# Kernel tuning notes

Measured on AMD Instinct MI355X. Metric: run time of the kernel, lower is better.

The kernel has to match this reference:

```python
import jax, jax.numpy as jnp
import numpy as np

EMBED_DIM = 1024
NUM_HEADS = 16
HEAD_DIM = EMBED_DIM // NUM_HEADS
B, N = 4, 2048


def setup_inputs() -> dict:
    key = jax.random.key(0)
    k = jax.random.split(key, 5)
    scale = 1.0 / np.sqrt(EMBED_DIM)
    return {
        "x": jax.random.normal(k[0], (B, N, EMBED_DIM), dtype=jnp.float32),
        # torch nn.Linear convention: y = x @ W.T + b, W shape [out, in]
        "qkv_w": jax.random.uniform(k[1], (3 * EMBED_DIM, EMBED_DIM), jnp.float32, -scale, scale),
        "qkv_b": jax.random.uniform(k[2], (3 * EMBED_DIM,), jnp.float32, -scale, scale),
        "out_w": jax.random.uniform(k[3], (EMBED_DIM, EMBED_DIM), jnp.float32, -scale, scale),
        "out_b": jax.random.uniform(k[4], (EMBED_DIM,), jnp.float32, -scale, scale),
    }


def reference(x, qkv_w, qkv_b, out_w, out_b):
    b, n, e = x.shape
    qkv = x @ qkv_w.T + qkv_b                      # [B,N,3E]
    qkv = qkv.reshape(b, n, 3, NUM_HEADS, HEAD_DIM)
    qkv = jnp.transpose(qkv, (2, 0, 3, 1, 4))      # [3,B,H,N,D]
    q, k, v = qkv[0], qkv[1], qkv[2]
    scores = jnp.einsum("bhqd,bhkd->bhqk", q, k) / np.sqrt(HEAD_DIM)
    weights = jax.nn.softmax(scores, axis=-1)
    attn = jnp.einsum("bhqk,bhkd->bhqd", weights, v)  # [B,H,N,D]
    attn = jnp.transpose(attn, (0, 2, 1, 3)).reshape(b, n, e)
    return attn @ out_w.T + out_b
```

## Files before the change

### kernel.cpp

```cpp
#include <hip/hip_runtime.h>
#include <hip/hip_bf16.h>

#define EMBED 1024
#define NHEADS 16
#define HDIM 64
#define BATCH 4
#define SEQ 2048
#define MROWS (BATCH*SEQ)
#define QKVN (3*EMBED)
#define KDIM 1024

typedef __bf16 bf16;
typedef __bf16 bf16x4 __attribute__((ext_vector_type(4)));
typedef __bf16 bf16x8 __attribute__((ext_vector_type(8)));
typedef float f32x4 __attribute__((ext_vector_type(4)));
typedef float f32x16 __attribute__((ext_vector_type(16)));

#define QSCALE 0.18033688011112042f

#define NX (MROWS*EMBED/4)
#define NQ (QKVN*KDIM/4)
#define NO (EMBED*KDIM/4)
__global__ void cvt_all(const float* __restrict__ x, const float* __restrict__ qw,
                        const float* __restrict__ ow,
                        bf16* __restrict__ xb, bf16* __restrict__ qwb, bf16* __restrict__ owb) {
    int i = blockIdx.x * blockDim.x + threadIdx.x;
    const float* src; bf16* dst; int j;
    if (i < NX)            { src = x;  dst = xb;  j = i; }
    else if (i < NX + NQ)  { src = qw; dst = qwb; j = i - NX; }
    else if (i < NX+NQ+NO) { src = ow; dst = owb; j = i - NX - NQ; }
    else return;
    float4 f = ((const float4*)src)[j];
    bf16x4 o;
    o[0] = (bf16)f.x; o[1] = (bf16)f.y; o[2] = (bf16)f.z; o[3] = (bf16)f.w;
    *((bf16x4*)dst + j) = o;
}

template<int MODE>
__launch_bounds__(256)
__global__ void gemm_bt(const bf16* __restrict__ A, const bf16* __restrict__ B,
                        const float* __restrict__ bias,
                        float* __restrict__ outF,
                        bf16* __restrict__ Qb, bf16* __restrict__ Kb, bf16* __restrict__ Vt)
{
    __shared__ __align__(16) char ldsmem[16384];
    bf16 (*Alds)[32] = (bf16(*)[32])ldsmem;
    bf16 (*Blds)[32] = (bf16(*)[32])(ldsmem + 8192);
    bf16* bounce = (bf16*)ldsmem;

    const int tid = threadIdx.x;
    const int l = tid & 63, w = tid >> 6;
    const int wr = w >> 1, wc = w & 1;
    const int tM = blockIdx.y * 128, tN = blockIdx.x * 128;

    f32x4 acc[4][4] = {};
    const bf16* Abase = A + (size_t)tM * KDIM;
    const bf16* Bbase = B + (size_t)tN * KDIM;

    for (int k0 = 0; k0 < KDIM; k0 += 32) {
        #pragma unroll
        for (int t = 0; t < 2; ++t) {
            int idx = t * 256 + tid;
            int row = idx >> 2;
            int kc = (idx & 3) * 8;
            __builtin_amdgcn_global_load_lds(
                (const __attribute__((address_space(1))) void*)(Abase + (size_t)row * KDIM + k0 + kc),
                (__attribute__((address_space(3))) void*)((char*)&Alds[0][0] + idx * 16),
                16, 0, 0);
            __builtin_amdgcn_global_load_lds(
                (const __attribute__((address_space(1))) void*)(Bbase + (size_t)row * KDIM + k0 + kc),
                (__attribute__((address_space(3))) void*)((char*)&Blds[0][0] + idx * 16),
                16, 0, 0);
        }
        __syncthreads();
        bf16x8 a[4], b[4];
        #pragma unroll
        for (int i = 0; i < 4; ++i)
            a[i] = *(const bf16x8*)&Alds[wr * 64 + i * 16 + (l & 15)][(l >> 4) * 8];
        #pragma unroll
        for (int j = 0; j < 4; ++j)
            b[j] = *(const bf16x8*)&Blds[wc * 64 + j * 16 + (l & 15)][(l >> 4) * 8];
        #pragma unroll
        for (int i = 0; i < 4; ++i)
            #pragma unroll
            for (int j = 0; j < 4; ++j)
                acc[i][j] = __builtin_amdgcn_mfma_f32_16x16x32_bf16(a[i], b[j], acc[i][j], 0, 0, 0);
        __syncthreads();
    }

    if (MODE == 1) {
        #pragma unroll
        for (int i = 0; i < 4; ++i) {
            #pragma unroll
            for (int j = 0; j < 4; ++j) {
                int n = tN + wc * 64 + j * 16 + (l & 15);
                float bv = bias[n];
                #pragma unroll
                for (int r = 0; r < 4; ++r) {
                    int m = tM + wr * 64 + i * 16 + (l >> 4) * 4 + r;
                    outF[(size_t)m * EMBED + n] = acc[i][j][r] + bv;
                }
            }
        }
    } else {
        const int which = tN >> 10;
        const int bidx  = tM >> 11;
        const int hd0   = (tN & 1023) >> 6;
        const int t32base = (tM & 2047) >> 5;
        bf16* dstbase = (which == 0) ? Qb : (which == 1) ? Kb : Vt;
        const float scale = (which == 0) ? QSCALE : 1.0f;

        float bj[4];
        #pragma unroll
        for (int j = 0; j < 4; ++j)
            bj[j] = bias[tN + wc * 64 + j * 16 + (l & 15)];

        #pragma unroll
        for (int pass = 0; pass < 2; ++pass) {
            __syncthreads();
            #pragma unroll
            for (int ii = 0; ii < 2; ++ii) {
                const int i = pass * 2 + ii;
                #pragma unroll
                for (int j = 0; j < 4; ++j) {
                    const int d = (wc * 64 + j * 16 + (l & 15)) & 63;
                    #pragma unroll
                    for (int r = 0; r < 4; ++r) {
                        const int nsl = wr * 64 + i * 16 + (l >> 4) * 4 + r;
                        float v = acc[i][j][r] + bj[j];
                        int off;
                        if (which == 2) {
                            int dblk = d >> 5;
                            int rem16 = nsl & 15;
                            int c = (nsl >> 4) & 1;
                            int fj = (rem16 & 3) | ((rem16 & 8) >> 1);
                            int fhi = (rem16 >> 2) & 1;
                            int lane = (d & 31) | (fhi << 5);
                            off = (dblk * 2 + c) * 512 + lane * 8 + fj;
                        } else {
                            int kk = d >> 4, fhi = (d >> 3) & 1, fj = d & 7;
                            int lane = (nsl & 31) | (fhi << 5);
                            off = kk * 512 + lane * 8 + fj;
                        }
                        bounce[(wc * 2 + wr) * 2048 + off] = (bf16)(v * scale);
                    }
                }
            }
            __syncthreads();
            const int chunk = tid >> 6;
            size_t gbase = ((size_t)(bidx * NHEADS + hd0 + (chunk >> 1)) * 64
                            + t32base + 2 * (chunk & 1) + pass) * 2048;
            #pragma unroll
            for (int s = 0; s < 4; ++s) {
                int eoff = s * 512 + (tid & 63) * 8;
                *(bf16x8*)(dstbase + gbase + eoff) = *(const bf16x8*)&bounce[chunk * 2048 + eoff];
            }
        }
    }
}

static __device__ __forceinline__ unsigned cvt_pk(float lo, float hi) {
    unsigned r;
    asm("v_cvt_pk_bf16_f32 %0, %1, %2" : "=v"(r) : "v"(lo), "v"(hi));
    return r;
}

__launch_bounds__(256)
__global__ void attn_kernel(const bf16* __restrict__ Qb, const bf16* __restrict__ Kb,
                            const bf16* __restrict__ Vt, bf16* __restrict__ AO)
{
    const int tid = threadIdx.x, l = tid & 63, w = tid >> 6;
    const int lo5 = l & 31, hi = l >> 5;
    int bid = blockIdx.x;
    int swz = (bid & 7) * 128 + (bid >> 3);
    const int bh = swz >> 4;
    const int qt = swz & 15;

    const bf16* QFh = Qb + (size_t)bh * (64 * 2048);
    const bf16* Kit = Kb + (size_t)bh * (64 * 2048) + (size_t)l * 8;
    const bf16* Vit = Vt + (size_t)bh * (64 * 2048) + (size_t)l * 8;

    const int qtile = qt * 4 + w;
    const bf16* qbase = QFh + (size_t)qtile * 2048 + (size_t)l * 8;
    bf16x8 qf[4];
    #pragma unroll
    for (int kk = 0; kk < 4; ++kk)
        qf[kk] = *(const bf16x8*)(qbase + kk * 512);

    f32x16 O0 = {}, O1 = {};
    float lsum = 0.f;

    bf16x8 vA00 = *(const bf16x8*)(Vit);
    bf16x8 vA01 = *(const bf16x8*)(Vit + 512);
    bf16x8 vA10 = *(const bf16x8*)(Vit + 1024);
    bf16x8 vA11 = *(const bf16x8*)(Vit + 1536);
    bf16x8 vB00, vB01, vB10, vB11;

    bf16x8 kK0 = *(const bf16x8*)(Kit);
    bf16x8 kK1 = *(const bf16x8*)(Kit + 512);
    bf16x8 kK2 = *(const bf16x8*)(Kit + 1024);
    bf16x8 kK3 = *(const bf16x8*)(Kit + 1536);

    f32x16 SA, SB;
    #pragma unroll
    for (int r = 0; r < 16; ++r) SA[r] = 0.f;
    SA = __builtin_amdgcn_mfma_f32_32x32x16_bf16(kK0, qf[0], SA, 0, 0, 0);
    SA = __builtin_amdgcn_mfma_f32_32x32x16_bf16(kK1, qf[1], SA, 0, 0, 0);
    SA = __builtin_amdgcn_mfma_f32_32x32x16_bf16(kK2, qf[2], SA, 0, 0, 0);
    SA = __builtin_amdgcn_mfma_f32_32x32x16_bf16(kK3, qf[3], SA, 0, 0, 0);
    kK0 = *(const bf16x8*)(Kit + 2048);
    kK1 = *(const bf16x8*)(Kit + 2048 + 512);
    kK2 = *(const bf16x8*)(Kit + 2048 + 1024);
    kK3 = *(const bf16x8*)(Kit + 2048 + 1536);

#define ATTN_BODY(T, SCUR, SNXT, VC00, VC01, VC10, VC11, VN00, VN01, VN10, VN11)        \
    {                                                                                    \
        const int t = (T);                                                               \
        int tv = t + 1; tv = (tv < 64) ? tv : 0;                                         \
        const bf16* vb = Vit + (size_t)tv * 2048;                                        \
        VN00 = *(const bf16x8*)(vb);                                                     \
        VN01 = *(const bf16x8*)(vb + 512);                                               \
        VN10 = *(const bf16x8*)(vb + 1024);                                              \
        VN11 = *(const bf16x8*)(vb + 1536);                                              \
        __builtin_amdgcn_s_setprio(1);                                                   \
        _Pragma("unroll")                                                                \
        for (int r = 0; r < 16; ++r) SNXT[r] = 0.f;                                      \
        SNXT = __builtin_amdgcn_mfma_f32_32x32x16_bf16(kK0, qf[0], SNXT, 0, 0, 0);       \
        SNXT = __builtin_amdgcn_mfma_f32_32x32x16_bf16(kK1, qf[1], SNXT, 0, 0, 0);       \
        SNXT = __builtin_amdgcn_mfma_f32_32x32x16_bf16(kK2, qf[2], SNXT, 0, 0, 0);       \
        SNXT = __builtin_amdgcn_mfma_f32_32x32x16_bf16(kK3, qf[3], SNXT, 0, 0, 0);       \
        __builtin_amdgcn_s_setprio(0);                                                   \
        int tp = t + 2; tp = (tp < 64) ? tp : 0;                                         \
        const bf16* kb = Kit + (size_t)tp * 2048;                                        \
        kK0 = *(const bf16x8*)(kb);                                                      \
        kK1 = *(const bf16x8*)(kb + 512);                                                \
        kK2 = *(const bf16x8*)(kb + 1024);                                               \
        kK3 = *(const bf16x8*)(kb + 1536);                                               \
        float p[16];                                                                     \
        _Pragma("unroll")                                                                \
        for (int r = 0; r < 16; ++r)                                                     \
            p[r] = __builtin_amdgcn_exp2f(SCUR[r]);                                      \
        float s0 = (p[0] + p[1]) + (p[2] + p[3]);                                        \
        float s1 = (p[4] + p[5]) + (p[6] + p[7]);                                        \
        float s2 = (p[8] + p[9]) + (p[10] + p[11]);                                      \
        float s3 = (p[12] + p[13]) + (p[14] + p[15]);                                    \
        lsum += (s0 + s1) + (s2 + s3);                                                   \
        union { unsigned u[4]; bf16x8 v; } pk0, pk1;                                     \
        pk0.u[0] = cvt_pk(p[0], p[1]);   pk0.u[1] = cvt_pk(p[2], p[3]);                  \
        pk0.u[2] = cvt_pk(p[4], p[5]);   pk0.u[3] = cvt_pk(p[6], p[7]);                  \
        pk1.u[0] = cvt_pk(p[8], p[9]);   pk1.u[1] = cvt_pk(p[10], p[11]);                \
        pk1.u[2] = cvt_pk(p[12], p[13]); pk1.u[3] = cvt_pk(p[14], p[15]);                \
        __builtin_amdgcn_s_setprio(1);                                                   \
        O0 = __builtin_amdgcn_mfma_f32_32x32x16_bf16(VC00, pk0.v, O0, 0, 0, 0);          \
        O0 = __builtin_amdgcn_mfma_f32_32x32x16_bf16(VC01, pk1.v, O0, 0, 0, 0);          \
        O1 = __builtin_amdgcn_mfma_f32_32x32x16_bf16(VC10, pk0.v, O1, 0, 0, 0);          \
        O1 = __builtin_amdgcn_mfma_f32_32x32x16_bf16(VC11, pk1.v, O1, 0, 0, 0);          \
        __builtin_amdgcn_s_setprio(0);                                                   \
    }

    for (int t2 = 0; t2 < 64; t2 += 2) {
        ATTN_BODY(t2,     SA, SB, vA00, vA01, vA10, vA11, vB00, vB01, vB10, vB11)
        ATTN_BODY(t2 + 1, SB, SA, vB00, vB01, vB10, vB11, vA00, vA01, vA10, vA11)
    }
#undef ATTN_BODY

    lsum += __shfl_xor(lsum, 32);
    float linv = 1.0f / lsum;

    const int b = bh >> 4, hd = bh & 15;
    const int q0 = qt * 128 + w * 32;
    bf16* outp = &AO[(size_t)(b * SEQ + q0 + lo5) * EMBED + hd * HDIM];
    #pragma unroll
    for (int g = 0; g < 4; ++g) {
        bf16x4 o0, o1;
        #pragma unroll
        for (int r4 = 0; r4 < 4; ++r4) {
            o0[r4] = (bf16)(O0[g * 4 + r4] * linv);
            o1[r4] = (bf16)(O1[g * 4 + r4] * linv);
        }
        *(bf16x4*)&outp[g * 8 + hi * 4] = o0;
        *(bf16x4*)&outp[32 + g * 8 + hi * 4] = o1;
    }
}

extern "C" void kernel_launch(void* const* d_in, const int* in_sizes, int n_in,
                              void* d_out, int out_size, void* d_ws, size_t ws_size,
                              hipStream_t stream) {
    const float* x     = (const float*)d_in[0];
    const float* qkv_w = (const float*)d_in[1];
    const float* qkv_b = (const float*)d_in[2];
    const float* out_w = (const float*)d_in[3];
    const float* out_b = (const float*)d_in[4];
    float* out = (float*)d_out;

    char* ws = (char*)d_ws;
    bf16* xb  = (bf16*)(ws);
    bf16* qwb = (bf16*)(ws + 16777216);
    bf16* owb = (bf16*)(ws + 23068672);
    bf16* Qb  = (bf16*)(ws + 25165824);
    bf16* Kb  = (bf16*)(ws + 41943040);
    bf16* Vt  = (bf16*)(ws + 58720256);
    bf16* AO  = (bf16*)(ws + 75497472);

    cvt_all<<<(NX + NQ + NO + 255) / 256, 256, 0, stream>>>(x, qkv_w, out_w, xb, qwb, owb);

    gemm_bt<0><<<dim3(QKVN / 128, MROWS / 128), 256, 0, stream>>>(
        xb, qwb, qkv_b, nullptr, Qb, Kb, Vt);

    attn_kernel<<<BATCH * NHEADS * (SEQ / 128), 256, 0, stream>>>(Qb, Kb, Vt, AO);

    gemm_bt<1><<<dim3(EMBED / 128, MROWS / 128), 256, 0, stream>>>(
        AO, owb, out_b, out, nullptr, nullptr, nullptr);
}
```

Before: 200.7 us.

## Use 64x128-tile GEMM for output projection and simplify attention K/V loads

Replaces the output-projection GEMM with a new kernel that uses 64x128 tiles, loads directly into LDS via global_load_lds and runs 16x16x32 MFMAs. This doubles the block count so work spreads more evenly across CUs. The attention loop now loads V for the current step instead of prefetching it one step ahead, advances K/V pointers incrementally, and seeds the score MFMA with a constant zero accumulator to save register-zeroing work. In exchange, V load latency is less hidden, the new GEMM has no double buffering, and the K prefetch now reads past the head's data on the final iterations instead of wrapping to the start.

```diff
diff --git a/kernel.cpp b/kernel.cpp
--- a/kernel.cpp
+++ b/kernel.cpp
@@ -159,6 +159,70 @@
     }
 }
 
+__launch_bounds__(256)
+__global__ void gemm_bt64(const bf16* __restrict__ A, const bf16* __restrict__ B,
+                          const float* __restrict__ bias, float* __restrict__ outF)
+{
+    __shared__ bf16 Alds[64][32];
+    __shared__ bf16 Blds[128][32];
+    const int tid = threadIdx.x;
+    const int l = tid & 63, w = tid >> 6;
+    const int tM = blockIdx.y * 64, tN = blockIdx.x * 128;
+
+    f32x4 acc[4][2] = {};
+    const bf16* Abase = A + (size_t)tM * KDIM;
+    const bf16* Bbase = B + (size_t)tN * KDIM;
+
+    for (int k0 = 0; k0 < KDIM; k0 += 32) {
+        {
+            int row = tid >> 2;
+            int kc = (tid & 3) * 8;
+            __builtin_amdgcn_global_load_lds(
+                (const __attribute__((address_space(1))) void*)(Abase + (size_t)row * KDIM + k0 + kc),
+                (__attribute__((address_space(3))) void*)((char*)&Alds[0][0] + tid * 16),
+                16, 0, 0);
+        }
+        #pragma unroll
+        for (int t = 0; t < 2; ++t) {
+            int idx = t * 256 + tid;
+            int row = idx >> 2;
+            int kc = (idx & 3) * 8;
+            __builtin_amdgcn_global_load_lds(
+                (const __attribute__((address_space(1))) void*)(Bbase + (size_t)row * KDIM + k0 + kc),
+                (__attribute__((address_space(3))) void*)((char*)&Blds[0][0] + idx * 16),
+                16, 0, 0);
+        }
+        __syncthreads();
+        bf16x8 a[4], b[2];
+        #pragma unroll
+        for (int i = 0; i < 4; ++i)
+            a[i] = *(const bf16x8*)&Alds[i * 16 + (l & 15)][(l >> 4) * 8];
+        #pragma unroll
+        for (int j = 0; j < 2; ++j)
+            b[j] = *(const bf16x8*)&Blds[w * 32 + j * 16 + (l & 15)][(l >> 4) * 8];
+        #pragma unroll
+        for (int i = 0; i < 4; ++i)
+            #pragma unroll
+            for (int j = 0; j < 2; ++j)
+                acc[i][j] = __builtin_amdgcn_mfma_f32_16x16x32_bf16(a[i], b[j], acc[i][j], 0, 0, 0);
+        __syncthreads();
+    }
+
+    #pragma unroll
+    for (int i = 0; i < 4; ++i) {
+        #pragma unroll
+        for (int j = 0; j < 2; ++j) {
+            int n = tN + w * 32 + j * 16 + (l & 15);
+            float bv = bias[n];
+            #pragma unroll
+            for (int r = 0; r < 4; ++r) {
+                int m = tM + i * 16 + (l >> 4) * 4 + r;
+                outF[(size_t)m * EMBED + n] = acc[i][j][r] + bv;
+            }
+        }
+    }
+}
+
 static __device__ __forceinline__ unsigned cvt_pk(float lo, float hi) {
     unsigned r;
     asm("v_cvt_pk_bf16_f32 %0, %1, %2" : "=v"(r) : "v"(lo), "v"(hi));
@@ -189,22 +253,14 @@
 
     f32x16 O0 = {}, O1 = {};
     float lsum = 0.f;
-
-    bf16x8 vA00 = *(const bf16x8*)(Vit);
-    bf16x8 vA01 = *(const bf16x8*)(Vit + 512);
-    bf16x8 vA10 = *(const bf16x8*)(Vit + 1024);
-    bf16x8 vA11 = *(const bf16x8*)(Vit + 1536);
-    bf16x8 vB00, vB01, vB10, vB11;
+    const f32x16 ZR = {};
 
     bf16x8 kK0 = *(const bf16x8*)(Kit);
     bf16x8 kK1 = *(const bf16x8*)(Kit + 512);
     bf16x8 kK2 = *(const bf16x8*)(Kit + 1024);
     bf16x8 kK3 = *(const bf16x8*)(Kit + 1536);
-
     f32x16 SA, SB;
-    #pragma unroll
-    for (int r = 0; r < 16; ++r) SA[r] = 0.f;
-    SA = __builtin_amdgcn_mfma_f32_32x32x16_bf16(kK0, qf[0], SA, 0, 0, 0);
+    SA = __builtin_amdgcn_mfma_f32_32x32x16_bf16(kK0, qf[0], ZR, 0, 0, 0);
     SA = __builtin_amdgcn_mfma_f32_32x32x16_bf16(kK1, qf[1], SA, 0, 0, 0);
     SA = __builtin_amdgcn_mfma_f32_32x32x16_bf16(kK2, qf[2], SA, 0, 0, 0);
     SA = __builtin_amdgcn_mfma_f32_32x32x16_bf16(kK3, qf[3], SA, 0, 0, 0);
@@ -213,29 +269,27 @@
     kK2 = *(const bf16x8*)(Kit + 2048 + 1024);
     kK3 = *(const bf16x8*)(Kit + 2048 + 1536);
 
-#define ATTN_BODY(T, SCUR, SNXT, VC00, VC01, VC10, VC11, VN00, VN01, VN10, VN11)        \
+    const bf16* kptr = Kit + 2 * 2048;
+    const bf16* vptr = Vit;
+
+#define ATTN_BODY(SCUR, SNXT)                                                            \
     {                                                                                    \
-        const int t = (T);                                                               \
-        int tv = t + 1; tv = (tv < 64) ? tv : 0;                                         \
-        const bf16* vb = Vit + (size_t)tv * 2048;                                        \
-        VN00 = *(const bf16x8*)(vb);                                                     \
-        VN01 = *(const bf16x8*)(vb + 512);                                               \
-        VN10 = *(const bf16x8*)(vb + 1024);                                              \
-        VN11 = *(const bf16x8*)(vb + 1536);                                              \
+        bf16x8 vf00 = *(const bf16x8*)(vptr);                                            \
+        bf16x8 vf01 = *(const bf16x8*)(vptr + 512);                                      \
+        bf16x8 vf10 = *(const bf16x8*)(vptr + 1024);                                     \
+        bf16x8 vf11 = *(const bf16x8*)(vptr + 1536);                                     \
+        vptr += 2048;                                                                    \
         __builtin_amdgcn_s_setprio(1);                                                   \
-        _Pragma("unroll")                                                                \
-        for (int r = 0; r < 16; ++r) SNXT[r] = 0.f;                                      \
-        SNXT = __builtin_amdgcn_mfma_f32_32x32x16_bf16(kK0, qf[0], SNXT, 0, 0, 0);       \
+        SNXT = __builtin_amdgcn_mfma_f32_32x32x16_bf16(kK0, qf[0], ZR, 0, 0, 0);         \
         SNXT = __builtin_amdgcn_mfma_f32_32x32x16_bf16(kK1, qf[1], SNXT, 0, 0, 0);       \
         SNXT = __builtin_amdgcn_mfma_f32_32x32x16_bf16(kK2, qf[2], SNXT, 0, 0, 0);       \
         SNXT = __builtin_amdgcn_mfma_f32_32x32x16_bf16(kK3, qf[3], SNXT, 0, 0, 0);       \
         __builtin_amdgcn_s_setprio(0);                                                   \
-        int tp = t + 2; tp = (tp < 64) ? tp : 0;                                         \
-        const bf16* kb = Kit + (size_t)tp * 2048;                                        \
-        kK0 = *(const bf16x8*)(kb);                                                      \
-        kK1 = *(const bf16x8*)(kb + 512);                                                \
-        kK2 = *(const bf16x8*)(kb + 1024);                                               \
-        kK3 = *(const bf16x8*)(kb + 1536);                                               \
+        kK0 = *(const bf16x8*)(kptr);                                                    \
+        kK1 = *(const bf16x8*)(kptr + 512);                                              \
+        kK2 = *(const bf16x8*)(kptr + 1024);                                             \
+        kK3 = *(const bf16x8*)(kptr + 1536);                                             \
+        kptr += 2048;                                                                    \
         float p[16];                                                                     \
         _Pragma("unroll")                                                                \
         for (int r = 0; r < 16; ++r)                                                     \
@@ -251,16 +305,16 @@
         pk1.u[0] = cvt_pk(p[8], p[9]);   pk1.u[1] = cvt_pk(p[10], p[11]);                \
         pk1.u[2] = cvt_pk(p[12], p[13]); pk1.u[3] = cvt_pk(p[14], p[15]);                \
         __builtin_amdgcn_s_setprio(1);                                                   \
-        O0 = __builtin_amdgcn_mfma_f32_32x32x16_bf16(VC00, pk0.v, O0, 0, 0, 0);          \
-        O0 = __builtin_amdgcn_mfma_f32_32x32x16_bf16(VC01, pk1.v, O0, 0, 0, 0);          \
-        O1 = __builtin_amdgcn_mfma_f32_32x32x16_bf16(VC10, pk0.v, O1, 0, 0, 0);          \
-        O1 = __builtin_amdgcn_mfma_f32_32x32x16_bf16(VC11, pk1.v, O1, 0, 0, 0);          \
+        O0 = __builtin_amdgcn_mfma_f32_32x32x16_bf16(vf00, pk0.v, O0, 0, 0, 0);          \
+        O0 = __builtin_amdgcn_mfma_f32_32x32x16_bf16(vf01, pk1.v, O0, 0, 0, 0);          \
+        O1 = __builtin_amdgcn_mfma_f32_32x32x16_bf16(vf10, pk0.v, O1, 0, 0, 0);          \
+        O1 = __builtin_amdgcn_mfma_f32_32x32x16_bf16(vf11, pk1.v, O1, 0, 0, 0);          \
         __builtin_amdgcn_s_setprio(0);                                                   \
     }
 
     for (int t2 = 0; t2 < 64; t2 += 2) {
-        ATTN_BODY(t2,     SA, SB, vA00, vA01, vA10, vA11, vB00, vB01, vB10, vB11)
-        ATTN_BODY(t2 + 1, SB, SA, vB00, vB01, vB10, vB11, vA00, vA01, vA10, vA11)
+        ATTN_BODY(SA, SB)
+        ATTN_BODY(SB, SA)
     }
 #undef ATTN_BODY
 
@@ -309,6 +363,5 @@
 
     attn_kernel<<<BATCH * NHEADS * (SEQ / 128), 256, 0, stream>>>(Qb, Kb, Vt, AO);
 
-    gemm_bt<1><<<dim3(EMBED / 128, MROWS / 128), 256, 0, stream>>>(
-        AO, owb, out_b, out, nullptr, nullptr, nullptr);
-}
+    gemm_bt64<<<dim3(EMBED / 128, MROWS / 64), 256, 0, stream>>>(AO, owb, out_b, out);
+}
```

New measurement: 205.7 us. 2.5% more time.
